# Performance work log

Measured on AMD Instinct MI355X. Metric: run time of the kernel, lower is better.

The kernel has to match this reference:

```python
import jax, jax.numpy as jnp
import numpy as np

N = 50000      # nodes
E = 800000     # edges (before self loops)
DIN = 128      # input feature dim
H = 2          # attention heads
C = 64         # per-head hidden channels (hidden_dim)
HC = H * C     # 128, concat output width of each GATv2 layer
DOUT = 4       # NUM_LANES
NEG = 0.2      # GATv2 default negative_slope


def _w(key, fan_in, shape):
    return jax.random.normal(key, shape, dtype=jnp.float32) * (1.0 / np.sqrt(fan_in))


def setup_inputs() -> dict:
    key = jax.random.key(0)
    ks = jax.random.split(key, 32)
    inp = {
        "x": jax.random.normal(ks[0], (N, DIN), dtype=jnp.float32),
        "edge_index": jax.random.randint(ks[1], (2, E), 0, N, dtype=jnp.int64),
    }
    # layer 1: DIN -> H*C
    inp["W1l"] = _w(ks[2], DIN, (DIN, HC)); inp["b1l"] = jnp.zeros((HC,), jnp.float32)
    inp["W1r"] = _w(ks[3], DIN, (DIN, HC)); inp["b1r"] = jnp.zeros((HC,), jnp.float32)
    inp["att1"] = _w(ks[4], C, (H, C));     inp["bias1"] = jnp.zeros((HC,), jnp.float32)
    # layer 2: H*C -> H*C
    inp["W2l"] = _w(ks[5], HC, (HC, HC));   inp["b2l"] = jnp.zeros((HC,), jnp.float32)
    inp["W2r"] = _w(ks[6], HC, (HC, HC));   inp["b2r"] = jnp.zeros((HC,), jnp.float32)
    inp["att2"] = _w(ks[7], C, (H, C));     inp["bias2"] = jnp.zeros((HC,), jnp.float32)
    # layer 3: H*C -> H*C
    inp["W3l"] = _w(ks[8], HC, (HC, HC));   inp["b3l"] = jnp.zeros((HC,), jnp.float32)
    inp["W3r"] = _w(ks[9], HC, (HC, HC));   inp["b3r"] = jnp.zeros((HC,), jnp.float32)
    inp["att3"] = _w(ks[10], C, (H, C));    inp["bias3"] = jnp.zeros((HC,), jnp.float32)
    # output linear
    inp["Wout"] = _w(ks[11], HC, (HC, DOUT)); inp["bout"] = jnp.zeros((DOUT,), jnp.float32)
    return inp


def gat_layer(x, src, dst, Wl, bl, Wr, br, att, bias):
    # GATv2Conv, concat=True, add_self_loops already in src/dst.
    n = x.shape[0]
    h, c = att.shape
    xl = (x @ Wl + bl).reshape(n, h, c)   # source transform
    xr = (x @ Wr + br).reshape(n, h, c)   # target transform
    m = xl[src] + xr[dst]                               # [Etot, H, C]
    e = jnp.sum(jax.nn.leaky_relu(m, NEG) * att, -1)    # [Etot, H]
    emax = jax.ops.segment_max(e, dst, num_segments=n)  # segment softmax over in-edges
    p = jnp.exp(e - emax[dst])
    denom = jax.ops.segment_sum(p, dst, num_segments=n)
    alpha = p / denom[dst]                              # [Etot, H]
    out = jax.ops.segment_sum(alpha[:, :, None] * xl[src], dst, num_segments=n)
    return out.reshape(n, h * c) + bias


def reference(x, edge_index, W1l, b1l, W1r, b1r, att1, bias1,
              W2l, b2l, W2r, b2r, att2, bias2,
              W3l, b3l, W3r, b3r, att3, bias3, Wout, bout):
    n = x.shape[0]
    loop = jnp.arange(n, dtype=edge_index.dtype)
    src = jnp.concatenate([edge_index[0], loop])  # add self loops (PyG default)
    dst = jnp.concatenate([edge_index[1], loop])
    h = jax.nn.relu(gat_layer(x, src, dst, W1l, b1l, W1r, b1r, att1, bias1))
    h = jax.nn.relu(gat_layer(h, src, dst, W2l, b2l, W2r, b2r, att2, bias2))
    h = jax.nn.relu(gat_layer(h, src, dst, W3l, b3l, W3r, b3r, att3, bias3))
    return h @ Wout + bout
```

## Files before the change

kernel.cpp:

```cpp
#include <hip/hip_runtime.h>
#include <math.h>

#define DIN  128
#define HC   128
#define NEG  0.2f

typedef __attribute__((ext_vector_type(8))) short bf16x8;
typedef __attribute__((ext_vector_type(4))) float f32x4;
typedef __attribute__((ext_vector_type(8))) _Float16 half8;

__device__ __forceinline__ unsigned short f2bf_rne(float x) {
    unsigned u = __float_as_uint(x);
    unsigned r = u + 0x7FFFu + ((u >> 16) & 1u);
    return (unsigned short)(r >> 16);
}
__device__ __forceinline__ float bf2f(unsigned short h) {
    return __uint_as_float(((unsigned)h) << 16);
}

template <int CTRL>
__device__ __forceinline__ float dpp_xadd(float x) {
    int r = __builtin_amdgcn_update_dpp(0, __float_as_int(x), CTRL, 0xF, 0xF, true);
    return x + __int_as_float(r);
}
__device__ __forceinline__ float rowsum16(float x) {
    x = dpp_xadd<0xB1>(x);
    x = dpp_xadd<0x4E>(x);
    x = dpp_xadd<0x141>(x);
    x = dpp_xadd<0x140>(x);
    return x;
}

__global__ void hist_kernel(const int* __restrict__ ei, int E, int N,
                            int* __restrict__ counts) {
    int i = blockIdx.x * blockDim.x + threadIdx.x;
    int Etot = E + N;
    if (i >= Etot) return;
    int dst = (i < E) ? ei[E + i] : (i - E);
    if (dst < 0 || dst >= N) return;
    atomicAdd(&counts[dst], 1);
}

__global__ void scan_kernel(const int* __restrict__ counts,
                            int* __restrict__ rowptr,
                            int* __restrict__ cursor, int n) {
    __shared__ int wsum[16];
    int tid  = threadIdx.x;
    int lane = tid & 63, wid = tid >> 6;
    int running = 0;
    for (int base = 0; base < n; base += 4096) {
        int i = base + tid * 4;
        int4 v = make_int4(0, 0, 0, 0);
        if (i < n) v = *(const int4*)&counts[i];
        int ssum = v.x + v.y + v.z + v.w;
        int x = ssum;
        #pragma unroll
        for (int off = 1; off < 64; off <<= 1) {
            int y = __shfl_up(x, off, 64);
            if (lane >= off) x += y;
        }
        if (lane == 63) wsum[wid] = x;
        __syncthreads();
        if (tid < 16) {
            int w = wsum[tid];
            #pragma unroll
            for (int off = 1; off < 16; off <<= 1) {
                int y = __shfl_up(w, off, 64);
                if (tid >= off) w += y;
            }
            wsum[tid] = w;
        }
        __syncthreads();
        int excl = running + (wid ? wsum[wid - 1] : 0) + (x - ssum);
        if (i < n) {
            int4 r;
            r.x = excl;
            r.y = r.x + v.x;
            r.z = r.y + v.y;
            r.w = r.z + v.z;
            *(int4*)&rowptr[i] = r;
            *(int4*)&cursor[i] = r;
        }
        running += wsum[15];
        __syncthreads();
    }
    if (tid == 0) rowptr[n] = running;
}

__global__ void scatter_kernel(const int* __restrict__ ei, int E, int N,
                               int* __restrict__ cursor,
                               int* __restrict__ esrc) {
    int i = blockIdx.x * blockDim.x + threadIdx.x;
    int Etot = E + N;
    if (i >= Etot) return;
    int src = (i < E) ? ei[i]     : (i - E);
    int dst = (i < E) ? ei[E + i] : (i - E);
    if (dst < 0 || dst >= N || src < 0 || src >= N) return;
    int pos = atomicAdd(&cursor[dst], 1);
    esrc[pos] = src;
}

__global__ __launch_bounds__(256) void prep_w(
        const float* __restrict__ W1l, const float* __restrict__ W1r,
        const float* __restrict__ W2l, const float* __restrict__ W2r,
        const float* __restrict__ W3l, const float* __restrict__ W3r,
        unsigned short* __restrict__ hi, unsigned short* __restrict__ lo) {
    int m = blockIdx.y;
    const float* W = (m == 0) ? W1l : (m == 1) ? W1r : (m == 2) ? W2l
                   : (m == 3) ? W2r : (m == 4) ? W3l : W3r;
    int t = blockIdx.x * 256 + threadIdx.x;
    int kb = t >> 9, nf = (t >> 6) & 7, l = t & 63;
    int col = nf * 16 + (l & 15);
    int k0  = kb * 32 + (l >> 4) * 8;
    size_t ob = ((size_t)m * 2048 + t) * 8;
    #pragma unroll
    for (int j = 0; j < 8; ++j) {
        float v = W[(size_t)(k0 + j) * 128 + col];
        unsigned short h = f2bf_rne(v);
        hi[ob + j] = h;
        lo[ob + j] = f2bf_rne(v - bf2f(h));
    }
}

__global__ __launch_bounds__(256) void gemm_mfma_dual(
        const float* __restrict__ X,
        const unsigned short* __restrict__ Whi,
        const unsigned short* __restrict__ Wlo, int matbase,
        const float* __restrict__ bl, const float* __restrict__ br,
        _Float16* __restrict__ xlh, _Float16* __restrict__ xrh, int nrows) {
    const unsigned short* hpl = Whi + ((size_t)(matbase + 0) * 16384);
    const unsigned short* lpl = Wlo + ((size_t)(matbase + 0) * 16384);
    const unsigned short* hpr = Whi + ((size_t)(matbase + 1) * 16384);
    const unsigned short* lpr = Wlo + ((size_t)(matbase + 1) * 16384);

    int w   = threadIdx.x >> 6;
    int l   = threadIdx.x & 63;
    int m15 = l & 15, g = l >> 4;
    int rowbase = blockIdx.x * 64 + w * 16;

    f32x4 accl[8], accr[8];
    #pragma unroll
    for (int nf = 0; nf < 8; ++nf) {
        accl[nf] = (f32x4){0.f, 0.f, 0.f, 0.f};
        accr[nf] = (f32x4){0.f, 0.f, 0.f, 0.f};
    }

    #pragma unroll
    for (int kb = 0; kb < 4; ++kb) {
        int arow = rowbase + m15;
        float4 x0 = make_float4(0.f, 0.f, 0.f, 0.f), x1 = x0;
        if (arow < nrows) {
            const float* xp = &X[(size_t)arow * 128 + kb * 32 + g * 8];
            x0 = *(const float4*)xp;
            x1 = *(const float4*)(xp + 4);
        }
        float xv[8] = {x0.x, x0.y, x0.z, x0.w, x1.x, x1.y, x1.z, x1.w};
        bf16x8 ahi, alo;
        #pragma unroll
        for (int j = 0; j < 8; ++j) {
            unsigned short h = f2bf_rne(xv[j]);
            ahi[j] = (short)h;
            alo[j] = (short)f2bf_rne(xv[j] - bf2f(h));
        }
        #pragma unroll
        for (int nf = 0; nf < 8; ++nf) {
            size_t off = (((size_t)kb * 8 + nf) * 64 + l) * 8;
            bf16x8 bhl = *(const bf16x8*)&hpl[off];
            bf16x8 bll = *(const bf16x8*)&lpl[off];
            bf16x8 bhr = *(const bf16x8*)&hpr[off];
            bf16x8 blr = *(const bf16x8*)&lpr[off];
            accl[nf] = __builtin_amdgcn_mfma_f32_16x16x32_bf16(ahi, bhl, accl[nf], 0, 0, 0);
            accl[nf] = __builtin_amdgcn_mfma_f32_16x16x32_bf16(ahi, bll, accl[nf], 0, 0, 0);
            accl[nf] = __builtin_amdgcn_mfma_f32_16x16x32_bf16(alo, bhl, accl[nf], 0, 0, 0);
            accr[nf] = __builtin_amdgcn_mfma_f32_16x16x32_bf16(ahi, bhr, accr[nf], 0, 0, 0);
            accr[nf] = __builtin_amdgcn_mfma_f32_16x16x32_bf16(ahi, blr, accr[nf], 0, 0, 0);
            accr[nf] = __builtin_amdgcn_mfma_f32_16x16x32_bf16(alo, bhr, accr[nf], 0, 0, 0);
        }
    }

    #pragma unroll
    for (int nf = 0; nf < 8; ++nf) {
        int col = nf * 16 + m15;
        int newpos = ((nf & 3) * 4 + (m15 >> 2)) * 8 + (nf >> 2) * 4 + (m15 & 3);
        float vbl = bl[col];
        float vbr = br[col];
        #pragma unroll
        for (int r = 0; r < 4; ++r) {
            int row = rowbase + g * 4 + r;
            if (row < nrows) {
                xlh[(size_t)row * 128 + newpos] = (_Float16)(accl[nf][r] + vbl);
                xrh[(size_t)row * 128 + newpos] = (_Float16)(accr[nf][r] + vbr);
            }
        }
    }
}

__device__ __forceinline__ float dsel(float4 a, float4 x, float4 tp, float4 tn) {
    float r, v;
    v = a.x + x.x; r  = v * (v > 0.f ? tp.x : tn.x);
    v = a.y + x.y; r += v * (v > 0.f ? tp.y : tn.y);
    v = a.z + x.z; r += v * (v > 0.f ? tp.z : tn.z);
    v = a.w + x.w; r += v * (v > 0.f ? tp.w : tn.w);
    return r;
}

__global__ __launch_bounds__(256) void gat_aggregate(
        const _Float16* __restrict__ xlh, const _Float16* __restrict__ xrh,
        const int* __restrict__ rowptr, const int* __restrict__ esrc,
        const float* __restrict__ att, const float* __restrict__ bias,
        float* __restrict__ hout, int n, int do_relu,
        const float* __restrict__ Wout, const float* __restrict__ bout,
        float* __restrict__ out4) {
    int node = (int)((blockIdx.x * blockDim.x + threadIdx.x) >> 6);
    int lane = threadIdx.x & 63;
    if (node >= n) return;
    int g  = lane >> 4;
    int gl = lane & 15;
    int c0 = gl * 4;

    half8 xrh8 = *(const half8*)&xrh[(size_t)node * 128 + gl * 8];
    float4 xr0 = make_float4((float)xrh8[0], (float)xrh8[1],
                             (float)xrh8[2], (float)xrh8[3]);
    float4 xr1 = make_float4((float)xrh8[4], (float)xrh8[5],
                             (float)xrh8[6], (float)xrh8[7]);
    float4 atp0 = *(const float4*)&att[c0];
    float4 atp1 = *(const float4*)&att[64 + c0];
    float4 atn0 = make_float4(NEG * atp0.x, NEG * atp0.y, NEG * atp0.z, NEG * atp0.w);
    float4 atn1 = make_float4(NEG * atp1.x, NEG * atp1.y, NEG * atp1.z, NEG * atp1.w);

    float s0 = 0.f, s1 = 0.f;
    float4 acc0 = make_float4(0.f, 0.f, 0.f, 0.f);
    float4 acc1 = make_float4(0.f, 0.f, 0.f, 0.f);

    int pbeg = rowptr[node], pend = rowptr[node + 1];
    int p = pbeg + g;
    bool v0 = p < pend;
    bool v1 = p + 4 < pend;
    half8 r0 = (half8)(_Float16)0.f, r1 = r0;
    if (v0) r0 = *(const half8*)&xlh[(size_t)esrc[p] * 128 + gl * 8];
    if (v1) r1 = *(const half8*)&xlh[(size_t)esrc[p + 4] * 128 + gl * 8];

    while (v0) {
        bool v2 = p + 8 < pend;
        half8 r2 = (half8)(_Float16)0.f;
        if (v2) r2 = *(const half8*)&xlh[(size_t)esrc[p + 8] * 128 + gl * 8];

        float4 a0 = make_float4((float)r0[0], (float)r0[1],
                                (float)r0[2], (float)r0[3]);
        float4 a1 = make_float4((float)r0[4], (float)r0[5],
                                (float)r0[6], (float)r0[7]);
        float t0 = rowsum16(dsel(a0, xr0, atp0, atn0));
        float t1 = rowsum16(dsel(a1, xr1, atp1, atn1));
        float p0 = __expf(fminf(t0, 80.f));
        float p1 = __expf(fminf(t1, 80.f));
        s0 += p0;  s1 += p1;
        acc0.x += p0 * a0.x;  acc0.y += p0 * a0.y;
        acc0.z += p0 * a0.z;  acc0.w += p0 * a0.w;
        acc1.x += p1 * a1.x;  acc1.y += p1 * a1.y;
        acc1.z += p1 * a1.z;  acc1.w += p1 * a1.w;

        r0 = r1; r1 = r2; v0 = v1; v1 = v2; p += 4;
    }

    #pragma unroll
    for (int off = 16; off <= 32; off <<= 1) {
        s0 += __shfl_xor(s0, off, 64);
        s1 += __shfl_xor(s1, off, 64);
        acc0.x += __shfl_xor(acc0.x, off, 64); acc0.y += __shfl_xor(acc0.y, off, 64);
        acc0.z += __shfl_xor(acc0.z, off, 64); acc0.w += __shfl_xor(acc0.w, off, 64);
        acc1.x += __shfl_xor(acc1.x, off, 64); acc1.y += __shfl_xor(acc1.y, off, 64);
        acc1.z += __shfl_xor(acc1.z, off, 64); acc1.w += __shfl_xor(acc1.w, off, 64);
    }

    float inv0 = 1.f / s0, inv1 = 1.f / s1;

    if (out4) {
        float o0[4], o1[4];
        float a0v[4] = {acc0.x, acc0.y, acc0.z, acc0.w};
        float a1v[4] = {acc1.x, acc1.y, acc1.z, acc1.w};
        #pragma unroll
        for (int i = 0; i < 4; ++i) {
            o0[i] = a0v[i] * inv0 + bias[c0 + i];
            o1[i] = a1v[i] * inv1 + bias[64 + c0 + i];
            if (do_relu) { o0[i] = fmaxf(o0[i], 0.f); o1[i] = fmaxf(o1[i], 0.f); }
        }
        float p0 = 0.f, p1 = 0.f, p2 = 0.f, p3 = 0.f;
        #pragma unroll
        for (int i = 0; i < 4; ++i) {
            float4 w = *(const float4*)&Wout[(c0 + i) * 4];
            p0 += o0[i] * w.x; p1 += o0[i] * w.y; p2 += o0[i] * w.z; p3 += o0[i] * w.w;
        }
        #pragma unroll
        for (int i = 0; i < 4; ++i) {
            float4 w = *(const float4*)&Wout[(64 + c0 + i) * 4];
            p0 += o1[i] * w.x; p1 += o1[i] * w.y; p2 += o1[i] * w.z; p3 += o1[i] * w.w;
        }
        p0 = rowsum16(p0); p1 = rowsum16(p1);
        p2 = rowsum16(p2); p3 = rowsum16(p3);
        if (lane == 0) {
            float4 o = make_float4(p0 + bout[0], p1 + bout[1],
                                   p2 + bout[2], p3 + bout[3]);
            *(float4*)&out4[(size_t)node * 4] = o;
        }
        return;
    }

    if (g == 0) {
        float4 vb = *(const float4*)&bias[c0];
        float4 o = make_float4(acc0.x * inv0 + vb.x, acc0.y * inv0 + vb.y,
                               acc0.z * inv0 + vb.z, acc0.w * inv0 + vb.w);
        if (do_relu) {
            o.x = fmaxf(o.x, 0.f); o.y = fmaxf(o.y, 0.f);
            o.z = fmaxf(o.z, 0.f); o.w = fmaxf(o.w, 0.f);
        }
        *(float4*)&hout[(size_t)node * 128 + c0] = o;
    } else if (g == 1) {
        float4 vb = *(const float4*)&bias[64 + c0];
        float4 o = make_float4(acc1.x * inv1 + vb.x, acc1.y * inv1 + vb.y,
                               acc1.z * inv1 + vb.z, acc1.w * inv1 + vb.w);
        if (do_relu) {
            o.x = fmaxf(o.x, 0.f); o.y = fmaxf(o.y, 0.f);
            o.z = fmaxf(o.z, 0.f); o.w = fmaxf(o.w, 0.f);
        }
        *(float4*)&hout[(size_t)node * 128 + 64 + c0] = o;
    }
}

extern "C" void kernel_launch(void* const* d_in, const int* in_sizes, int n_in,
                              void* d_out, int out_size, void* d_ws,
                              size_t ws_size, hipStream_t stream) {
    const float* x    = (const float*)d_in[0];
    const int*   ei   = (const int*)  d_in[1];
    const float* W1l  = (const float*)d_in[2];
    const float* b1l  = (const float*)d_in[3];
    const float* W1r  = (const float*)d_in[4];
    const float* b1r  = (const float*)d_in[5];
    const float* att1 = (const float*)d_in[6];
    const float* bias1= (const float*)d_in[7];
    const float* W2l  = (const float*)d_in[8];
    const float* b2l  = (const float*)d_in[9];
    const float* W2r  = (const float*)d_in[10];
    const float* b2r  = (const float*)d_in[11];
    const float* att2 = (const float*)d_in[12];
    const float* bias2= (const float*)d_in[13];
    const float* W3l  = (const float*)d_in[14];
    const float* b3l  = (const float*)d_in[15];
    const float* W3r  = (const float*)d_in[16];
    const float* b3r  = (const float*)d_in[17];
    const float* att3 = (const float*)d_in[18];
    const float* bias3= (const float*)d_in[19];
    const float* Wout = (const float*)d_in[20];
    const float* bout = (const float*)d_in[21];

    int N    = in_sizes[0] / DIN;
    int E    = in_sizes[1] / 2;
    int Etot = E + N;

    char* base = (char*)d_ws;
    float* h = (float*)base;              base += (size_t)N * HC * 4;
    _Float16* xlh = (_Float16*)base;      base += (size_t)N * HC * 2;
    _Float16* xrh = (_Float16*)base;      base += (size_t)N * HC * 2;
    unsigned short* whi = (unsigned short*)base;  base += 6 * 16384 * 2;
    unsigned short* wlo = (unsigned short*)base;  base += 6 * 16384 * 2;
    int* esrc   = (int*)base;             base += (size_t)Etot * 4;
    int* rowptr = (int*)base;             base += (size_t)(((N + 1) + 3) & ~3) * 4;
    int* cursor = (int*)base;             base += (size_t)N * 4;
    int* counts = (int*)base;

    hipMemsetAsync(counts, 0, (size_t)N * sizeof(int), stream);
    hist_kernel<<<(Etot + 255) / 256, 256, 0, stream>>>(ei, E, N, counts);
    scan_kernel<<<1, 1024, 0, stream>>>(counts, rowptr, cursor, N);
    scatter_kernel<<<(Etot + 255) / 256, 256, 0, stream>>>(ei, E, N, cursor, esrc);
    prep_w<<<dim3(8, 6), 256, 0, stream>>>(W1l, W1r, W2l, W2r, W3l, W3r, whi, wlo);

    int gemm_grid = (N + 63) / 64;
    int agg_grid  = (N + 3) / 4;

    gemm_mfma_dual<<<gemm_grid, 256, 0, stream>>>(x, whi, wlo, 0, b1l, b1r, xlh, xrh, N);
    gat_aggregate<<<agg_grid, 256, 0, stream>>>(xlh, xrh, rowptr, esrc, att1, bias1,
                                                h, N, 1, nullptr, nullptr, nullptr);
    gemm_mfma_dual<<<gemm_grid, 256, 0, stream>>>(h, whi, wlo, 2, b2l, b2r, xlh, xrh, N);
    gat_aggregate<<<agg_grid, 256, 0, stream>>>(xlh, xrh, rowptr, esrc, att2, bias2,
                                                h, N, 1, nullptr, nullptr, nullptr);
    gemm_mfma_dual<<<gemm_grid, 256, 0, stream>>>(h, whi, wlo, 4, b3l, b3r, xlh, xrh, N);
    gat_aggregate<<<agg_grid, 256, 0, stream>>>(xlh, xrh, rowptr, esrc, att3, bias3,
                                                nullptr, N, 1, Wout, bout,
                                                (float*)d_out);
}
```

Baseline: 392.3 us.

## Permute feature layout so each lane handles one head in aggregation

Changes the column order of the fp16 xl/xr buffers and hidden activations so that each 8-element chunk a lane loads belongs to a single attention head. Per edge, a lane then needs one 8-lane DPP reduction and one exp, where before it needed two 16-lane reductions and two exps for two heads. To keep the math correct, the row order of the layer 2 and 3 weights is permuted in prep_w, and the attention, bias and Wout lookups are remapped. The GEMM epilogue also writes packed half2 values instead of scalar halves. The cost is extra index arithmetic and a more fragile layout that the layers and the final projection must all agree on.

```diff
diff --git a/kernel.cpp b/kernel.cpp
--- a/kernel.cpp
+++ b/kernel.cpp
@@ -8,6 +8,7 @@
 typedef __attribute__((ext_vector_type(8))) short bf16x8;
 typedef __attribute__((ext_vector_type(4))) float f32x4;
 typedef __attribute__((ext_vector_type(8))) _Float16 half8;
+typedef __attribute__((ext_vector_type(2))) _Float16 half2v;
 
 __device__ __forceinline__ unsigned short f2bf_rne(float x) {
     unsigned u = __float_as_uint(x);
@@ -18,10 +19,20 @@
     return __uint_as_float(((unsigned)h) << 16);
 }
 
+__device__ __forceinline__ int colOf(int p) {
+    return ((p >> 5) * 2 + (p & 1)) * 16 + ((p & 31) >> 1);
+}
+
 template <int CTRL>
 __device__ __forceinline__ float dpp_xadd(float x) {
     int r = __builtin_amdgcn_update_dpp(0, __float_as_int(x), CTRL, 0xF, 0xF, true);
     return x + __int_as_float(r);
+}
+__device__ __forceinline__ float rowsum8(float x) {
+    x = dpp_xadd<0xB1>(x);
+    x = dpp_xadd<0x4E>(x);
+    x = dpp_xadd<0x141>(x);
+    return x;
 }
 __device__ __forceinline__ float rowsum16(float x) {
     x = dpp_xadd<0xB1>(x);
@@ -115,7 +126,9 @@
     size_t ob = ((size_t)m * 2048 + t) * 8;
     #pragma unroll
     for (int j = 0; j < 8; ++j) {
-        float v = W[(size_t)(k0 + j) * 128 + col];
+        int k = k0 + j;
+        int krow = (m >= 2) ? colOf(k) : k;
+        float v = W[(size_t)krow * 128 + col];
         unsigned short h = f2bf_rne(v);
         hi[ob + j] = h;
         lo[ob + j] = f2bf_rne(v - bf2f(h));
@@ -133,8 +146,9 @@
     const unsigned short* hpr = Whi + ((size_t)(matbase + 1) * 16384);
     const unsigned short* lpr = Wlo + ((size_t)(matbase + 1) * 16384);
 
-    int w   = threadIdx.x >> 6;
-    int l   = threadIdx.x & 63;
+    int tid = threadIdx.x;
+    int w   = tid >> 6;
+    int l   = tid & 63;
     int m15 = l & 15, g = l >> 4;
     int rowbase = blockIdx.x * 64 + w * 16;
 
@@ -178,30 +192,29 @@
         }
     }
 
+    float vbl[8], vbr[8];
     #pragma unroll
     for (int nf = 0; nf < 8; ++nf) {
-        int col = nf * 16 + m15;
-        int newpos = ((nf & 3) * 4 + (m15 >> 2)) * 8 + (nf >> 2) * 4 + (m15 & 3);
-        float vbl = bl[col];
-        float vbr = br[col];
+        vbl[nf] = bl[nf * 16 + m15];
+        vbr[nf] = br[nf * 16 + m15];
+    }
+
+    #pragma unroll
+    for (int a = 0; a < 4; ++a) {
         #pragma unroll
         for (int r = 0; r < 4; ++r) {
             int row = rowbase + g * 4 + r;
-            if (row < nrows) {
-                xlh[(size_t)row * 128 + newpos] = (_Float16)(accl[nf][r] + vbl);
-                xrh[(size_t)row * 128 + newpos] = (_Float16)(accr[nf][r] + vbr);
-            }
-        }
-    }
-}
-
-__device__ __forceinline__ float dsel(float4 a, float4 x, float4 tp, float4 tn) {
-    float r, v;
-    v = a.x + x.x; r  = v * (v > 0.f ? tp.x : tn.x);
-    v = a.y + x.y; r += v * (v > 0.f ? tp.y : tn.y);
-    v = a.z + x.z; r += v * (v > 0.f ? tp.z : tn.z);
-    v = a.w + x.w; r += v * (v > 0.f ? tp.w : tn.w);
-    return r;
+            if (row >= nrows) continue;
+            size_t off = (size_t)row * 128 + a * 32 + m15 * 2;
+            half2v pl, pr;
+            pl[0] = (_Float16)(accl[2 * a][r]     + vbl[2 * a]);
+            pl[1] = (_Float16)(accl[2 * a + 1][r] + vbl[2 * a + 1]);
+            pr[0] = (_Float16)(accr[2 * a][r]     + vbr[2 * a]);
+            pr[1] = (_Float16)(accr[2 * a + 1][r] + vbr[2 * a + 1]);
+            *(half2v*)&xlh[off] = pl;
+            *(half2v*)&xrh[off] = pr;
+        }
+    }
 }
 
 __global__ __launch_bounds__(256) void gat_aggregate(
@@ -214,115 +227,98 @@
     int node = (int)((blockIdx.x * blockDim.x + threadIdx.x) >> 6);
     int lane = threadIdx.x & 63;
     if (node >= n) return;
-    int g  = lane >> 4;
-    int gl = lane & 15;
-    int c0 = gl * 4;
-
-    half8 xrh8 = *(const half8*)&xrh[(size_t)node * 128 + gl * 8];
-    float4 xr0 = make_float4((float)xrh8[0], (float)xrh8[1],
-                             (float)xrh8[2], (float)xrh8[3]);
-    float4 xr1 = make_float4((float)xrh8[4], (float)xrh8[5],
-                             (float)xrh8[6], (float)xrh8[7]);
-    float4 atp0 = *(const float4*)&att[c0];
-    float4 atp1 = *(const float4*)&att[64 + c0];
-    float4 atn0 = make_float4(NEG * atp0.x, NEG * atp0.y, NEG * atp0.z, NEG * atp0.w);
-    float4 atn1 = make_float4(NEG * atp1.x, NEG * atp1.y, NEG * atp1.z, NEG * atp1.w);
-
-    float s0 = 0.f, s1 = 0.f;
-    float4 acc0 = make_float4(0.f, 0.f, 0.f, 0.f);
-    float4 acc1 = make_float4(0.f, 0.f, 0.f, 0.f);
+    int g    = lane >> 4;
+    int gl   = lane & 15;
+    int pos0 = gl * 8;
+
+    half8 xr8 = *(const half8*)&xrh[(size_t)node * 128 + pos0];
+    float xrf[8], atp[8], atn[8];
+    #pragma unroll
+    for (int i = 0; i < 8; ++i) {
+        float a = att[colOf(pos0 + i)];
+        atp[i] = a;
+        atn[i] = NEG * a;
+        xrf[i] = (float)xr8[i];
+    }
+
+    float s = 0.f;
+    float acc[8];
+    #pragma unroll
+    for (int i = 0; i < 8; ++i) acc[i] = 0.f;
 
     int pbeg = rowptr[node], pend = rowptr[node + 1];
     int p = pbeg + g;
     bool v0 = p < pend;
     bool v1 = p + 4 < pend;
     half8 r0 = (half8)(_Float16)0.f, r1 = r0;
-    if (v0) r0 = *(const half8*)&xlh[(size_t)esrc[p] * 128 + gl * 8];
-    if (v1) r1 = *(const half8*)&xlh[(size_t)esrc[p + 4] * 128 + gl * 8];
+    if (v0) r0 = *(const half8*)&xlh[(size_t)esrc[p] * 128 + pos0];
+    if (v1) r1 = *(const half8*)&xlh[(size_t)esrc[p + 4] * 128 + pos0];
 
     while (v0) {
         bool v2 = p + 8 < pend;
         half8 r2 = (half8)(_Float16)0.f;
-        if (v2) r2 = *(const half8*)&xlh[(size_t)esrc[p + 8] * 128 + gl * 8];
-
-        float4 a0 = make_float4((float)r0[0], (float)r0[1],
-                                (float)r0[2], (float)r0[3]);
-        float4 a1 = make_float4((float)r0[4], (float)r0[5],
-                                (float)r0[6], (float)r0[7]);
-        float t0 = rowsum16(dsel(a0, xr0, atp0, atn0));
-        float t1 = rowsum16(dsel(a1, xr1, atp1, atn1));
-        float p0 = __expf(fminf(t0, 80.f));
-        float p1 = __expf(fminf(t1, 80.f));
-        s0 += p0;  s1 += p1;
-        acc0.x += p0 * a0.x;  acc0.y += p0 * a0.y;
-        acc0.z += p0 * a0.z;  acc0.w += p0 * a0.w;
-        acc1.x += p1 * a1.x;  acc1.y += p1 * a1.y;
-        acc1.z += p1 * a1.z;  acc1.w += p1 * a1.w;
+        if (v2) r2 = *(const half8*)&xlh[(size_t)esrc[p + 8] * 128 + pos0];
+
+        float av[8], t = 0.f;
+        #pragma unroll
+        for (int i = 0; i < 8; ++i) {
+            av[i] = (float)r0[i];
+            float v = av[i] + xrf[i];
+            t += v * (v > 0.f ? atp[i] : atn[i]);
+        }
+        t = rowsum8(t);
+        float pp = __expf(fminf(t, 80.f));
+        s += pp;
+        #pragma unroll
+        for (int i = 0; i < 8; ++i) acc[i] += pp * av[i];
 
         r0 = r1; r1 = r2; v0 = v1; v1 = v2; p += 4;
     }
 
     #pragma unroll
     for (int off = 16; off <= 32; off <<= 1) {
-        s0 += __shfl_xor(s0, off, 64);
-        s1 += __shfl_xor(s1, off, 64);
-        acc0.x += __shfl_xor(acc0.x, off, 64); acc0.y += __shfl_xor(acc0.y, off, 64);
-        acc0.z += __shfl_xor(acc0.z, off, 64); acc0.w += __shfl_xor(acc0.w, off, 64);
-        acc1.x += __shfl_xor(acc1.x, off, 64); acc1.y += __shfl_xor(acc1.y, off, 64);
-        acc1.z += __shfl_xor(acc1.z, off, 64); acc1.w += __shfl_xor(acc1.w, off, 64);
-    }
-
-    float inv0 = 1.f / s0, inv1 = 1.f / s1;
+        s += __shfl_xor(s, off, 64);
+        #pragma unroll
+        for (int i = 0; i < 8; ++i) acc[i] += __shfl_xor(acc[i], off, 64);
+    }
+
+    float inv = 1.f / s;
 
     if (out4) {
-        float o0[4], o1[4];
-        float a0v[4] = {acc0.x, acc0.y, acc0.z, acc0.w};
-        float a1v[4] = {acc1.x, acc1.y, acc1.z, acc1.w};
-        #pragma unroll
-        for (int i = 0; i < 4; ++i) {
-            o0[i] = a0v[i] * inv0 + bias[c0 + i];
-            o1[i] = a1v[i] * inv1 + bias[64 + c0 + i];
-            if (do_relu) { o0[i] = fmaxf(o0[i], 0.f); o1[i] = fmaxf(o1[i], 0.f); }
+        float o[8];
+        #pragma unroll
+        for (int i = 0; i < 8; ++i) {
+            o[i] = acc[i] * inv + bias[colOf(pos0 + i)];
+            if (do_relu) o[i] = fmaxf(o[i], 0.f);
         }
         float p0 = 0.f, p1 = 0.f, p2 = 0.f, p3 = 0.f;
         #pragma unroll
-        for (int i = 0; i < 4; ++i) {
-            float4 w = *(const float4*)&Wout[(c0 + i) * 4];
-            p0 += o0[i] * w.x; p1 += o0[i] * w.y; p2 += o0[i] * w.z; p3 += o0[i] * w.w;
-        }
-        #pragma unroll
-        for (int i = 0; i < 4; ++i) {
-            float4 w = *(const float4*)&Wout[(64 + c0 + i) * 4];
-            p0 += o1[i] * w.x; p1 += o1[i] * w.y; p2 += o1[i] * w.z; p3 += o1[i] * w.w;
+        for (int i = 0; i < 8; ++i) {
+            float4 wv = *(const float4*)&Wout[colOf(pos0 + i) * 4];
+            p0 += o[i] * wv.x; p1 += o[i] * wv.y;
+            p2 += o[i] * wv.z; p3 += o[i] * wv.w;
         }
         p0 = rowsum16(p0); p1 = rowsum16(p1);
         p2 = rowsum16(p2); p3 = rowsum16(p3);
         if (lane == 0) {
-            float4 o = make_float4(p0 + bout[0], p1 + bout[1],
-                                   p2 + bout[2], p3 + bout[3]);
-            *(float4*)&out4[(size_t)node * 4] = o;
+            float4 ov = make_float4(p0 + bout[0], p1 + bout[1],
+                                    p2 + bout[2], p3 + bout[3]);
+            *(float4*)&out4[(size_t)node * 4] = ov;
         }
         return;
     }
 
     if (g == 0) {
-        float4 vb = *(const float4*)&bias[c0];
-        float4 o = make_float4(acc0.x * inv0 + vb.x, acc0.y * inv0 + vb.y,
-                               acc0.z * inv0 + vb.z, acc0.w * inv0 + vb.w);
-        if (do_relu) {
-            o.x = fmaxf(o.x, 0.f); o.y = fmaxf(o.y, 0.f);
-            o.z = fmaxf(o.z, 0.f); o.w = fmaxf(o.w, 0.f);
-        }
-        *(float4*)&hout[(size_t)node * 128 + c0] = o;
-    } else if (g == 1) {
-        float4 vb = *(const float4*)&bias[64 + c0];
-        float4 o = make_float4(acc1.x * inv1 + vb.x, acc1.y * inv1 + vb.y,
-                               acc1.z * inv1 + vb.z, acc1.w * inv1 + vb.w);
-        if (do_relu) {
-            o.x = fmaxf(o.x, 0.f); o.y = fmaxf(o.y, 0.f);
-            o.z = fmaxf(o.z, 0.f); o.w = fmaxf(o.w, 0.f);
-        }
-        *(float4*)&hout[(size_t)node * 128 + 64 + c0] = o;
+        float o[8];
+        #pragma unroll
+        for (int i = 0; i < 8; ++i) {
+            o[i] = acc[i] * inv + bias[colOf(pos0 + i)];
+            if (do_relu) o[i] = fmaxf(o[i], 0.f);
+        }
+        float4 o0 = make_float4(o[0], o[1], o[2], o[3]);
+        float4 o1 = make_float4(o[4], o[5], o[6], o[7]);
+        *(float4*)&hout[(size_t)node * 128 + pos0]     = o0;
+        *(float4*)&hout[(size_t)node * 128 + pos0 + 4] = o1;
     }
 }
 
```

After: 361.5 us. 7.9% less time.
